# Kernel optimization log

Measured on AMD Instinct MI355X. Metric: run time of the kernel, lower is better.

Reference implementation:

```python
import jax, jax.numpy as jnp
import numpy as np
from jax import lax

B, S, F, K = 64, 1024, 256, 8  # batch, seq_len, features, kernel_size
L = S - K + 1                  # output sequence length (valid conv)


def setup_inputs() -> dict:
    key = jax.random.key(0)
    k1, k2 = jax.random.split(key)
    x = jax.random.normal(k1, (B, S, F), dtype=jnp.float32)
    # Conv1d weight [out_ch, in_ch, kernel], bias [out_ch]
    conv_w = jax.random.normal(k2, (F, F, K), dtype=jnp.float32) * 0.05
    conv_b = jnp.zeros((F,), dtype=jnp.float32)
    return {"x": x, "conv_w": conv_w, "conv_b": conv_b}


def reference(x, conv_w, conv_b):
    # tau = sigmoid(Conv1d(x.detach().T)).T  -> [B, L, F]
    xt = lax.stop_gradient(x).transpose(0, 2, 1)  # [B, F, S]
    t = lax.conv_general_dilated(
        xt, conv_w, window_strides=(1,), padding="VALID",
        dimension_numbers=("NCH", "OIH", "NCH"))
    tau = jax.nn.sigmoid(t + conv_b[None, :, None]).transpose(0, 2, 1)  # [B, L, F]

    # den = sum_{i=0}^{K-1} tau^i  (geometric series normalization)
    den = sum(tau ** i for i in range(K))
    # filter weights w_i = tau^(K-1-i) / den, stacked on window axis -> [B, L, K, F]
    w = jnp.stack([tau ** (K - 1 - i) for i in range(K)], axis=2) / den[:, :, None, :]

    # sliding windows of x: xw[b, l, i, f] = x[b, l+i, f]  -> [B, L, K, F]
    xw = jnp.stack([x[:, i:i + L, :] for i in range(K)], axis=2)

    # weighted window sum over kernel axis -> [B, L, F]
    return jnp.sum(w * xw, axis=2)
```

## Files before the change

kernel.cpp:

```cpp
#include <hip/hip_runtime.h>
#include <cmath>

#define BB 64
#define SS 1024
#define FF 256
#define KK 8
#define LL 1017

#define CC 64
#define RS 136

typedef __attribute__((ext_vector_type(8))) short bf16x8;
typedef __attribute__((ext_vector_type(8))) short short8v;
typedef __attribute__((ext_vector_type(16))) float f32x16;

__device__ __forceinline__ short f2bf(float f) {
  unsigned u = __float_as_uint(f);
  unsigned r = (u + 0x7fffu + ((u >> 16) & 1u)) >> 16;
  return (short)r;
}
__device__ __forceinline__ float bf2f(short s) {
  return __uint_as_float(((unsigned)(unsigned short)s) << 16);
}

__global__ __launch_bounds__(256) void convert_x_kernel(
    const float* __restrict__ x, short* __restrict__ xh,
    short* __restrict__ xl) {
  const int e0 = (blockIdx.x * 256 + threadIdx.x) * 8;
  const float4 v0 = *(const float4*)&x[e0];
  const float4 v1 = *(const float4*)&x[e0 + 4];
  const float vv[8] = {v0.x, v0.y, v0.z, v0.w, v1.x, v1.y, v1.z, v1.w};
  short8v hv, lv;
#pragma unroll
  for (int j = 0; j < 8; ++j) {
    const short h = f2bf(vv[j]);
    hv[j] = h;
    lv[j] = f2bf(vv[j] - bf2f(h));
  }
  *(short8v*)&xh[e0] = hv;
  *(short8v*)&xl[e0] = lv;
}

__global__ __launch_bounds__(256) void pack_w_kernel(
    const float* __restrict__ w, short* __restrict__ wh,
    short* __restrict__ wl) {
  const int e = blockIdx.x * 256 + threadIdx.x;
  const int T = e >> 12;
  const int n = (e >> 4) & 255;
  const int gj = e & 15;
  const int i = ((T & 15) << 4) + gj;
  const int k = T >> 4;
  const float v = w[n * 2048 + i * 8 + k];
  const short h = f2bf(v);
  wh[e] = h;
  wl[e] = f2bf(v - bf2f(h));
}

__global__ __launch_bounds__(256, 3) void gemm_mfma_kernel(
    const short* __restrict__ xh, const short* __restrict__ xl,
    const short* __restrict__ wh, const short* __restrict__ wl,
    const float* __restrict__ x, const float* __restrict__ cb,
    float* __restrict__ out) {
  __shared__ __align__(16) char smem[2 * RS * CC * 2];
  short* xsh = (short*)smem;
  short* xsl = (short*)(smem + RS * CC * 2);
  float(*ts)[132] = (float(*)[132])smem;

  const int tid = threadIdx.x;
  const int lane = tid & 63;
  const int wid = tid >> 6;
  const int wm = wid >> 1, wn = wid & 1;
  const int l5 = lane & 31, hi = lane >> 5;

  const int bx0 = blockIdx.x;
  const int bx = (bx0 & 7) * 128 + (bx0 >> 3);
  const int b = bx >> 4;
  const int rem = bx & 15;
  const int l0 = (rem >> 1) * 128;
  const int o0 = (rem & 1) * 128;

  f32x16 acc[2][2];
#pragma unroll
  for (int p = 0; p < 2; ++p)
#pragma unroll
    for (int q = 0; q < 2; ++q) acc[p][q] = (f32x16)0.f;

  const short* xhb = xh + b * (SS * FF);
  const short* xlb = xl + b * (SS * FF);

  const int srow = lane >> 3;
  const int sslot = lane & 7;

  for (int c = 0; c < 4; ++c) {
    const int cbase = c * CC;
    __syncthreads();
    for (int idx = wid; idx < 34; idx += 4) {
      const int arr = idx >= 17 ? 1 : 0;
      const int rb = arr ? idx - 17 : idx;
      const int row = rb * 8 + srow;
      int gr = l0 + row;
      gr = gr > (SS - 1) ? (SS - 1) : gr;
      const int slot_swz = sslot ^ (row & 7);
      const short* gsrc =
          (arr ? xlb : xhb) + gr * FF + cbase + slot_swz * 8;
      char* ldst = (arr ? (char*)xsl : (char*)xsh) + rb * 1024;
      __builtin_amdgcn_global_load_lds(
          (const __attribute__((address_space(1))) unsigned*)gsrc,
          (__attribute__((address_space(3))) unsigned*)ldst, 16, 0, 0);
    }
    __syncthreads();

#pragma unroll
    for (int k = 0; k < 8; ++k) {
#pragma unroll
      for (int i2 = 0; i2 < 4; ++i2) {
        const int T = k * 16 + c * 4 + i2;
        const int i0loc = i2 * 16;
        bf16x8 ah[2], al[2], bhf[2], blf[2];
#pragma unroll
        for (int p = 0; p < 2; ++p) {
          const int row = wm * 64 + p * 32 + l5 + k;
          int byte = row * 128 + (i0loc + hi * 8) * 2;
          byte ^= (row & 7) << 4;
          ah[p] = *(const bf16x8*)((const char*)xsh + byte);
          al[p] = *(const bf16x8*)((const char*)xsl + byte);
        }
#pragma unroll
        for (int q = 0; q < 2; ++q) {
          const int n = o0 + wn * 64 + q * 32 + l5;
          const int off = T * 4096 + n * 16 + hi * 8;
          bhf[q] = *(const bf16x8*)(wh + off);
          blf[q] = *(const bf16x8*)(wl + off);
        }
#pragma unroll
        for (int p = 0; p < 2; ++p)
#pragma unroll
          for (int q = 0; q < 2; ++q) {
            acc[p][q] = __builtin_amdgcn_mfma_f32_32x32x16_bf16(
                al[p], bhf[q], acc[p][q], 0, 0, 0);
            acc[p][q] = __builtin_amdgcn_mfma_f32_32x32x16_bf16(
                ah[p], blf[q], acc[p][q], 0, 0, 0);
            acc[p][q] = __builtin_amdgcn_mfma_f32_32x32x16_bf16(
                ah[p], bhf[q], acc[p][q], 0, 0, 0);
          }
      }
    }
  }

  const float* xb = x + b * (SS * FF);
  float* ob = out + (size_t)b * LL * FF;
  const int c0 = (tid & 31) * 4;
  const int rr0 = (tid >> 5) * 8;
  float bias4[4];
  *(float4*)&bias4[0] = *(const float4*)&cb[o0 + c0];

  for (int ph = 0; ph < 2; ++ph) {
    __syncthreads();
    if (wm == ph) {
#pragma unroll
      for (int p = 0; p < 2; ++p)
#pragma unroll
        for (int q = 0; q < 2; ++q)
#pragma unroll
          for (int r = 0; r < 16; ++r)
            ts[p * 32 + (r & 3) + 8 * (r >> 2) + 4 * hi]
              [wn * 64 + q * 32 + l5] = acc[p][q][r];
    }
    __syncthreads();

    const int grow = l0 + ph * 64 + rr0;
    float4 win[8];
#pragma unroll
    for (int s = 0; s < 7; ++s) {
      int rr = grow + s;
      rr = rr > (SS - 1) ? (SS - 1) : rr;
      win[s] = *(const float4*)&xb[rr * FF + o0 + c0];
    }
#pragma unroll
    for (int r = 0; r < 8; ++r) {
      int rr = grow + r + 7;
      rr = rr > (SS - 1) ? (SS - 1) : rr;
      win[(r + 7) & 7] = *(const float4*)&xb[rr * FF + o0 + c0];

      const float4 tv4 = *(const float4*)&ts[rr0 + r][c0];
      const float tvv[4] = {tv4.x, tv4.y, tv4.z, tv4.w};
      float num[4];
#pragma unroll
      for (int cq = 0; cq < 4; ++cq) {
        const float tt = 1.f / (1.f + expf(-(tvv[cq] + bias4[cq])));
        float d = 1.f;
#pragma unroll
        for (int e = 0; e < 7; ++e) d = fmaf(d, tt, 1.f);
        float n = win[r & 7][cq];
#pragma unroll
        for (int i = 1; i < 8; ++i) n = fmaf(n, tt, win[(r + i) & 7][cq]);
        num[cq] = n / d;
      }
      const int l = grow + r;
      if (l < LL) {
        float4 o4 = {num[0], num[1], num[2], num[3]};
        *(float4*)&ob[(size_t)l * FF + o0 + c0] = o4;
      }
    }
  }
}

extern "C" void kernel_launch(void* const* d_in, const int* in_sizes, int n_in,
                              void* d_out, int out_size, void* d_ws,
                              size_t ws_size, hipStream_t stream) {
  const float* x = (const float*)d_in[0];
  const float* w = (const float*)d_in[1];
  const float* cb = (const float*)d_in[2];
  float* out = (float*)d_out;

  const size_t NX = (size_t)BB * SS * FF;
  const size_t NW = 128ull * 4096ull;

  short* xh = (short*)d_ws;
  short* xl = xh + NX;
  short* wh = xl + NX;
  short* wl = wh + NW;

  convert_x_kernel<<<(int)(NX / (256 * 8)), 256, 0, stream>>>(x, xh, xl);
  pack_w_kernel<<<(int)(NW / 256), 256, 0, stream>>>(w, wh, wl);
  gemm_mfma_kernel<<<1024, 256, 0, stream>>>(xh, xl, wh, wl, x, cb, out);
}
```

Measured before the change: 346.2 us.

## Double-buffer LDS x-chunk staging and coalesce weight packing reads

The GEMM kernel now uses two LDS buffers. The next 64-channel chunk is prefetched with global_load_lds while the current one feeds the MFMAs, synchronised with explicit vmcnt waits and raw barriers. This is meant to hide global-load latency that was exposed between the two syncthreads per chunk. In exchange, doubled LDS lowers the occupancy hint from 3 to 2 blocks per CU. The weight-pack kernel is also reorganised to read contiguous float4s per thread, and the MFMAs are reordered into three grouped passes.

```diff
diff --git a/kernel.cpp b/kernel.cpp
--- a/kernel.cpp
+++ b/kernel.cpp
@@ -9,6 +9,7 @@
 
 #define CC 64
 #define RS 136
+#define BUFSZ (2 * RS * CC * 2)
 
 typedef __attribute__((ext_vector_type(8))) short bf16x8;
 typedef __attribute__((ext_vector_type(8))) short short8v;
@@ -44,26 +45,50 @@
 __global__ __launch_bounds__(256) void pack_w_kernel(
     const float* __restrict__ w, short* __restrict__ wh,
     short* __restrict__ wl) {
-  const int e = blockIdx.x * 256 + threadIdx.x;
-  const int T = e >> 12;
-  const int n = (e >> 4) & 255;
-  const int gj = e & 15;
-  const int i = ((T & 15) << 4) + gj;
-  const int k = T >> 4;
-  const float v = w[n * 2048 + i * 8 + k];
-  const short h = f2bf(v);
-  wh[e] = h;
-  wl[e] = f2bf(v - bf2f(h));
-}
-
-__global__ __launch_bounds__(256, 3) void gemm_mfma_kernel(
+  const int n = blockIdx.x;
+  const int i = threadIdx.x;
+  const float* src = w + n * 2048 + i * 8;
+  const float4 a = *(const float4*)src;
+  const float4 b = *(const float4*)(src + 4);
+  const float vv[8] = {a.x, a.y, a.z, a.w, b.x, b.y, b.z, b.w};
+  const int ihi = i >> 4;
+  const int slot = i & 15;
+#pragma unroll
+  for (int k = 0; k < 8; ++k) {
+    const int e = (k * 16 + ihi) * 4096 + n * 16 + slot;
+    const short h = f2bf(vv[k]);
+    wh[e] = h;
+    wl[e] = f2bf(vv[k] - bf2f(h));
+  }
+}
+
+__device__ __forceinline__ void stage_chunk(const short* xhb, const short* xlb,
+                                            char* bufbase, int cbase, int l0,
+                                            int wid, int srow, int sslot) {
+#pragma unroll
+  for (int jj = 0; jj < 9; ++jj) {
+    const int idx = wid + jj * 4;
+    const int arr = idx >= 18 ? 1 : 0;
+    int rb = arr ? idx - 18 : idx;
+    rb = rb > 16 ? 16 : rb;
+    const int row = rb * 8 + srow;
+    int gr = l0 + row;
+    gr = gr > (SS - 1) ? (SS - 1) : gr;
+    const int slot_swz = sslot ^ (row & 7);
+    const short* gsrc = (arr ? xlb : xhb) + gr * FF + cbase + slot_swz * 8;
+    char* ldst = bufbase + arr * (RS * CC * 2) + rb * 1024;
+    __builtin_amdgcn_global_load_lds(
+        (const __attribute__((address_space(1))) unsigned*)gsrc,
+        (__attribute__((address_space(3))) unsigned*)ldst, 16, 0, 0);
+  }
+}
+
+__global__ __launch_bounds__(256, 2) void gemm_mfma_kernel(
     const short* __restrict__ xh, const short* __restrict__ xl,
     const short* __restrict__ wh, const short* __restrict__ wl,
     const float* __restrict__ x, const float* __restrict__ cb,
     float* __restrict__ out) {
-  __shared__ __align__(16) char smem[2 * RS * CC * 2];
-  short* xsh = (short*)smem;
-  short* xsl = (short*)(smem + RS * CC * 2);
+  __shared__ __align__(16) char smem[2 * BUFSZ];
   float(*ts)[132] = (float(*)[132])smem;
 
   const int tid = threadIdx.x;
@@ -91,24 +116,23 @@
   const int srow = lane >> 3;
   const int sslot = lane & 7;
 
+  stage_chunk(xhb, xlb, smem, 0, l0, wid, srow, sslot);
+
+#pragma unroll
   for (int c = 0; c < 4; ++c) {
-    const int cbase = c * CC;
-    __syncthreads();
-    for (int idx = wid; idx < 34; idx += 4) {
-      const int arr = idx >= 17 ? 1 : 0;
-      const int rb = arr ? idx - 17 : idx;
-      const int row = rb * 8 + srow;
-      int gr = l0 + row;
-      gr = gr > (SS - 1) ? (SS - 1) : gr;
-      const int slot_swz = sslot ^ (row & 7);
-      const short* gsrc =
-          (arr ? xlb : xhb) + gr * FF + cbase + slot_swz * 8;
-      char* ldst = (arr ? (char*)xsl : (char*)xsh) + rb * 1024;
-      __builtin_amdgcn_global_load_lds(
-          (const __attribute__((address_space(1))) unsigned*)gsrc,
-          (__attribute__((address_space(3))) unsigned*)ldst, 16, 0, 0);
-    }
-    __syncthreads();
+    if (c > 0) __builtin_amdgcn_s_barrier();
+    if (c < 3) {
+      stage_chunk(xhb, xlb, smem + ((c + 1) & 1) * BUFSZ, (c + 1) * CC, l0,
+                  wid, srow, sslot);
+      asm volatile("s_waitcnt vmcnt(9)" ::: "memory");
+    } else {
+      asm volatile("s_waitcnt vmcnt(0)" ::: "memory");
+    }
+    __builtin_amdgcn_s_barrier();
+
+    const char* base = smem + (c & 1) * BUFSZ;
+    const short* xsh_c = (const short*)base;
+    const short* xsl_c = (const short*)(base + RS * CC * 2);
 
 #pragma unroll
     for (int k = 0; k < 8; ++k) {
@@ -122,8 +146,8 @@
           const int row = wm * 64 + p * 32 + l5 + k;
           int byte = row * 128 + (i0loc + hi * 8) * 2;
           byte ^= (row & 7) << 4;
-          ah[p] = *(const bf16x8*)((const char*)xsh + byte);
-          al[p] = *(const bf16x8*)((const char*)xsl + byte);
+          ah[p] = *(const bf16x8*)((const char*)xsh_c + byte);
+          al[p] = *(const bf16x8*)((const char*)xsl_c + byte);
         }
 #pragma unroll
         for (int q = 0; q < 2; ++q) {
@@ -133,16 +157,17 @@
           blf[q] = *(const bf16x8*)(wl + off);
         }
 #pragma unroll
-        for (int p = 0; p < 2; ++p)
-#pragma unroll
-          for (int q = 0; q < 2; ++q) {
-            acc[p][q] = __builtin_amdgcn_mfma_f32_32x32x16_bf16(
-                al[p], bhf[q], acc[p][q], 0, 0, 0);
-            acc[p][q] = __builtin_amdgcn_mfma_f32_32x32x16_bf16(
-                ah[p], blf[q], acc[p][q], 0, 0, 0);
-            acc[p][q] = __builtin_amdgcn_mfma_f32_32x32x16_bf16(
-                ah[p], bhf[q], acc[p][q], 0, 0, 0);
-          }
+        for (int pq = 0; pq < 4; ++pq)
+          acc[pq >> 1][pq & 1] = __builtin_amdgcn_mfma_f32_32x32x16_bf16(
+              al[pq >> 1], bhf[pq & 1], acc[pq >> 1][pq & 1], 0, 0, 0);
+#pragma unroll
+        for (int pq = 0; pq < 4; ++pq)
+          acc[pq >> 1][pq & 1] = __builtin_amdgcn_mfma_f32_32x32x16_bf16(
+              ah[pq >> 1], blf[pq & 1], acc[pq >> 1][pq & 1], 0, 0, 0);
+#pragma unroll
+        for (int pq = 0; pq < 4; ++pq)
+          acc[pq >> 1][pq & 1] = __builtin_amdgcn_mfma_f32_32x32x16_bf16(
+              ah[pq >> 1], bhf[pq & 1], acc[pq >> 1][pq & 1], 0, 0, 0);
       }
     }
   }
@@ -222,6 +247,6 @@
   short* wl = wh + NW;
 
   convert_x_kernel<<<(int)(NX / (256 * 8)), 256, 0, stream>>>(x, xh, xl);
-  pack_w_kernel<<<(int)(NW / 256), 256, 0, stream>>>(w, wh, wl);
+  pack_w_kernel<<<256, 256, 0, stream>>>(w, wh, wl);
   gemm_mfma_kernel<<<1024, 256, 0, stream>>>(xh, xl, wh, wl, x, cb, out);
 }
```

New measurement: 324.2 us. -6.4%, faster.
